# Optimization experiments

Hardware: AMD Instinct MI355X
Metric: run time of the kernel (lower is better)

Reference implementation:

```python
import jax, jax.numpy as jnp
import numpy as np

BS = 8192      # total agents (batch)
T = 8          # trajectory length
NB = 128       # number of sub-batches (crowd groups)
BLK = BS // NB # agents per group = 64
EPS = 1e-7


def setup_inputs() -> dict:
    key = jax.random.key(0)
    ks = jax.random.split(key, 7)
    x = jax.random.normal(ks[0], (BS, T, 2), dtype=jnp.float32)
    # Kaiming-ish scaled params matching nn.Linear fan-in
    W1 = jax.random.normal(ks[1], (2, 32), dtype=jnp.float32) / np.sqrt(2.0)
    b1 = jax.random.normal(ks[2], (32,), dtype=jnp.float32) * 0.01
    W2 = jax.random.normal(ks[3], (32, 64), dtype=jnp.float32) / np.sqrt(32.0)
    b2 = jax.random.normal(ks[4], (64,), dtype=jnp.float32) * 0.01
    W3 = jax.random.normal(ks[5], (64, 64), dtype=jnp.float32) / np.sqrt(64.0)
    b3 = jax.random.normal(ks[6], (64,), dtype=jnp.float32) * 0.01
    starts = jnp.arange(NB, dtype=jnp.int32) * BLK
    sub_batches = jnp.stack([starts, starts + BLK], axis=1)  # [NB, 2]
    return {"x": x, "W1": W1, "b1": b1, "W2": W2, "b2": b2,
            "W3": W3, "b3": b3, "sub_batches": sub_batches}


def reference(x, W1, b1, W2, b2, W3, b3, sub_batches):
    bs = x.shape[0]
    xt = x[:, -1]                                   # [bs, 2] last timestep
    h = jax.nn.relu(xt @ W1 + b1)                   # [bs, 32]
    h = jax.nn.relu(h @ W2 + b2)                    # [bs, 64]
    h = h @ W3 + b3                                 # [bs, 64]

    nb = sub_batches.shape[0]
    blk = bs // nb
    hb = h.reshape(nb, blk, -1)                     # [nb, blk, 64]
    attn = jnp.einsum('nid,njd->nij', hb, hb)       # [nb, blk, blk]
    # Faithful to torch: attn - attn.max(1)[0] broadcasts row-max m[j]
    # along the LAST axis (attn[i,j] - m[j]).
    m = attn.max(axis=2)                            # [nb, blk]
    e = jnp.exp(attn - m[:, None, :])
    blocks = e / (e.sum(axis=2, keepdims=True) + EPS)

    # Scatter normalized blocks onto the block diagonal of a zero bs x bs matrix
    rows = sub_batches[:, 0][:, None] + jnp.arange(blk)  # [nb, blk]
    attens = jnp.zeros((bs, bs), dtype=h.dtype)
    attens = attens.at[rows[:, :, None], rows[:, None, :]].set(blocks)
    return attens
```

## Files before the change

### kernel.cpp

```cpp
#include <hip/hip_runtime.h>

#define BS   8192
#define TT   8
#define NB   128
#define BLK  64
#define EPS  1e-7f

#define FILL_ITERS 16
#define NFILL      ((BS * (BS / 4)) / (256 * FILL_ITERS))

__global__ __launch_bounds__(256, 2) void attn_fused(
    const float* __restrict__ x,
    const float* __restrict__ W1, const float* __restrict__ b1,
    const float* __restrict__ W2, const float* __restrict__ b2,
    const float* __restrict__ W3, const float* __restrict__ b3,
    const int*   __restrict__ sub_batches,
    float* __restrict__ out)
{
    const int tid = threadIdx.x;
    const int bid = blockIdx.x;

    if (bid >= NB) {
        float4* __restrict__ out4 = (float4*)out;
        const float4 z = make_float4(0.f, 0.f, 0.f, 0.f);
        const int base = (bid - NB) * (256 * FILL_ITERS) + tid;
        #pragma unroll
        for (int it = 0; it < FILL_ITERS; ++it) {
            const int idx  = base + it * 256;
            const int row  = idx >> 11;
            const int col4 = idx & 2047;
            if ((col4 >> 4) != (row >> 6)) out4[idx] = z;
        }
        return;
    }

    __shared__ __align__(16) float sW2[32 * 64];
    __shared__ __align__(16) float sW3[64 * 64];
    __shared__ __align__(16) float h1[64][36];
    __shared__ __align__(16) float h2[64][68];
    __shared__ __align__(16) float h3[64][68];
    __shared__ float sW1[2 * 32];
    __shared__ float sb1[32];
    __shared__ float sb2[64];
    __shared__ float sb3[64];
    __shared__ float mcol[64];
    __shared__ float rsum[64][4];

    const int n     = bid;
    const int start = sub_batches[2 * n];

    for (int i = tid; i < 2 * 32; i += 256)  sW1[i] = W1[i];
    if (tid < 32)                            sb1[tid] = b1[tid];
    for (int i = tid; i < 32 * 64; i += 256) sW2[i] = W2[i];
    if (tid < 64)                            sb2[tid] = b2[tid];
    for (int i = tid; i < 64 * 64; i += 256) sW3[i] = W3[i];
    if (tid >= 64 && tid < 128)              sb3[tid - 64] = b3[tid - 64];
    __syncthreads();

    const int row = tid >> 2;
    const int f0  = (tid & 3) * 16;

    const int r = start + row;
    const float2 xv = *(const float2*)&x[((size_t)r * TT + (TT - 1)) * 2];

    {
        const int g0 = (tid & 3) * 8;
        #pragma unroll
        for (int f = 0; f < 8; ++f) {
            float v = fmaf(xv.x, sW1[g0 + f], fmaf(xv.y, sW1[32 + g0 + f], sb1[g0 + f]));
            h1[row][g0 + f] = fmaxf(v, 0.f);
        }
    }
    __syncthreads();

    {
        float acc[16];
        #pragma unroll
        for (int i = 0; i < 16; ++i) acc[i] = sb2[f0 + i];
        for (int k = 0; k < 32; ++k) {
            const float hk = h1[row][k];
            const float4* wp = (const float4*)&sW2[k * 64 + f0];
            #pragma unroll
            for (int c = 0; c < 4; ++c) {
                const float4 w = wp[c];
                acc[4*c+0] = fmaf(hk, w.x, acc[4*c+0]);
                acc[4*c+1] = fmaf(hk, w.y, acc[4*c+1]);
                acc[4*c+2] = fmaf(hk, w.z, acc[4*c+2]);
                acc[4*c+3] = fmaf(hk, w.w, acc[4*c+3]);
            }
        }
        #pragma unroll
        for (int c = 0; c < 4; ++c) {
            float4 v = make_float4(fmaxf(acc[4*c+0], 0.f), fmaxf(acc[4*c+1], 0.f),
                                   fmaxf(acc[4*c+2], 0.f), fmaxf(acc[4*c+3], 0.f));
            ((float4*)&h2[row][f0])[c] = v;
        }
    }
    __syncthreads();

    {
        float acc[16];
        #pragma unroll
        for (int i = 0; i < 16; ++i) acc[i] = sb3[f0 + i];
        for (int k = 0; k < 64; ++k) {
            const float hk = h2[row][k];
            const float4* wp = (const float4*)&sW3[k * 64 + f0];
            #pragma unroll
            for (int c = 0; c < 4; ++c) {
                const float4 w = wp[c];
                acc[4*c+0] = fmaf(hk, w.x, acc[4*c+0]);
                acc[4*c+1] = fmaf(hk, w.y, acc[4*c+1]);
                acc[4*c+2] = fmaf(hk, w.z, acc[4*c+2]);
                acc[4*c+3] = fmaf(hk, w.w, acc[4*c+3]);
            }
        }
        #pragma unroll
        for (int c = 0; c < 4; ++c) {
            ((float4*)&h3[row][f0])[c] =
                make_float4(acc[4*c+0], acc[4*c+1], acc[4*c+2], acc[4*c+3]);
        }
    }
    __syncthreads();

    float (*attn)[68] = h2;
    {
        float4 rv[16];
        const float4* rp = (const float4*)&h3[row][0];
        #pragma unroll
        for (int kk = 0; kk < 16; ++kk) rv[kk] = rp[kk];

        #pragma unroll
        for (int jj = 0; jj < 16; ++jj) {
            const int j = f0 + jj;
            const float4* vp = (const float4*)&h3[j][0];
            float s0 = 0.f, s1 = 0.f, s2 = 0.f, s3 = 0.f;
            #pragma unroll
            for (int kk = 0; kk < 16; ++kk) {
                const float4 v = vp[kk];
                s0 = fmaf(rv[kk].x, v.x, s0);
                s1 = fmaf(rv[kk].y, v.y, s1);
                s2 = fmaf(rv[kk].z, v.z, s2);
                s3 = fmaf(rv[kk].w, v.w, s3);
            }
            attn[row][j] = (s0 + s1) + (s2 + s3);
        }
    }
    __syncthreads();

    if (tid < 64) {
        const float4* ap = (const float4*)&attn[tid][0];
        float4 m4 = ap[0];
        #pragma unroll
        for (int kk = 1; kk < 16; ++kk) {
            const float4 v = ap[kk];
            m4.x = fmaxf(m4.x, v.x); m4.y = fmaxf(m4.y, v.y);
            m4.z = fmaxf(m4.z, v.z); m4.w = fmaxf(m4.w, v.w);
        }
        mcol[tid] = fmaxf(fmaxf(m4.x, m4.y), fmaxf(m4.z, m4.w));
    }
    __syncthreads();

    {
        float ps = 0.f;
        #pragma unroll
        for (int jj = 0; jj < 16; ++jj) {
            const int j = f0 + jj;
            const float e = expf(attn[row][j] - mcol[j]);
            attn[row][j] = e;
            ps += e;
        }
        rsum[row][tid & 3] = ps;
    }
    __syncthreads();

    const float s   = rsum[row][0] + rsum[row][1] + rsum[row][2] + rsum[row][3] + EPS;
    const float inv = 1.f / s;

    float4* ob = (float4*)(out + (size_t)(start + row) * BS + start + f0);
    #pragma unroll
    for (int c = 0; c < 4; ++c) {
        const float4 e4 = ((const float4*)&attn[row][f0])[c];
        ob[c] = make_float4(e4.x * inv, e4.y * inv, e4.z * inv, e4.w * inv);
    }
}

extern "C" void kernel_launch(void* const* d_in, const int* in_sizes, int n_in,
                              void* d_out, int out_size, void* d_ws, size_t ws_size,
                              hipStream_t stream) {
    const float* x   = (const float*)d_in[0];
    const float* W1  = (const float*)d_in[1];
    const float* b1  = (const float*)d_in[2];
    const float* W2  = (const float*)d_in[3];
    const float* b2  = (const float*)d_in[4];
    const float* W3  = (const float*)d_in[5];
    const float* b3  = (const float*)d_in[6];
    const int*   sb  = (const int*)d_in[7];
    float* out = (float*)d_out;

    attn_fused<<<NB + NFILL, 256, 0, stream>>>(x, W1, b1, W2, b2, W3, b3, sb, out);
}
```

Measured before the change: 265.3 us.

## Replace in-kernel zero fill with hipMemsetAsync and widen blocks to 512 threads

Drops the custom fill blocks that wrote zeros off the diagonal and instead clears the whole 256MB output with hipMemsetAsync before launching a block-only kernel. The block kernel now uses 512 threads, with each row split over 8 threads instead of 4, so each thread computes 8 features. This relies on the driver memset reaching full bandwidth, at the cost of writing the diagonal blocks twice and running a second launch serialized on the stream.

```diff
diff --git a/kernel.cpp b/kernel.cpp
--- a/kernel.cpp
+++ b/kernel.cpp
@@ -6,10 +6,7 @@
 #define BLK  64
 #define EPS  1e-7f
 
-#define FILL_ITERS 16
-#define NFILL      ((BS * (BS / 4)) / (256 * FILL_ITERS))
-
-__global__ __launch_bounds__(256, 2) void attn_fused(
+__global__ __launch_bounds__(512) void attn_blocks(
     const float* __restrict__ x,
     const float* __restrict__ W1, const float* __restrict__ b1,
     const float* __restrict__ W2, const float* __restrict__ b2,
@@ -17,23 +14,6 @@
     const int*   __restrict__ sub_batches,
     float* __restrict__ out)
 {
-    const int tid = threadIdx.x;
-    const int bid = blockIdx.x;
-
-    if (bid >= NB) {
-        float4* __restrict__ out4 = (float4*)out;
-        const float4 z = make_float4(0.f, 0.f, 0.f, 0.f);
-        const int base = (bid - NB) * (256 * FILL_ITERS) + tid;
-        #pragma unroll
-        for (int it = 0; it < FILL_ITERS; ++it) {
-            const int idx  = base + it * 256;
-            const int row  = idx >> 11;
-            const int col4 = idx & 2047;
-            if ((col4 >> 4) != (row >> 6)) out4[idx] = z;
-        }
-        return;
-    }
-
     __shared__ __align__(16) float sW2[32 * 64];
     __shared__ __align__(16) float sW3[64 * 64];
     __shared__ __align__(16) float h1[64][36];
@@ -44,29 +24,31 @@
     __shared__ float sb2[64];
     __shared__ float sb3[64];
     __shared__ float mcol[64];
-    __shared__ float rsum[64][4];
+    __shared__ float rsum[64][8];
 
-    const int n     = bid;
+    const int tid   = threadIdx.x;
+    const int n     = blockIdx.x;
     const int start = sub_batches[2 * n];
 
-    for (int i = tid; i < 2 * 32; i += 256)  sW1[i] = W1[i];
+    if (tid < 64)                            sW1[tid] = W1[tid];
     if (tid < 32)                            sb1[tid] = b1[tid];
-    for (int i = tid; i < 32 * 64; i += 256) sW2[i] = W2[i];
-    if (tid < 64)                            sb2[tid] = b2[tid];
-    for (int i = tid; i < 64 * 64; i += 256) sW3[i] = W3[i];
-    if (tid >= 64 && tid < 128)              sb3[tid - 64] = b3[tid - 64];
+    for (int i = tid; i < 32 * 64; i += 512) sW2[i] = W2[i];
+    if (tid >= 448)                          sb2[tid - 448] = b2[tid - 448];
+    for (int i = tid; i < 64 * 64; i += 512) sW3[i] = W3[i];
+    if (tid >= 384 && tid < 448)             sb3[tid - 384] = b3[tid - 384];
     __syncthreads();
 
-    const int row = tid >> 2;
-    const int f0  = (tid & 3) * 16;
+    const int row = tid >> 3;
+    const int l8  = tid & 7;
+    const int f0  = l8 * 8;
 
     const int r = start + row;
     const float2 xv = *(const float2*)&x[((size_t)r * TT + (TT - 1)) * 2];
 
     {
-        const int g0 = (tid & 3) * 8;
+        const int g0 = l8 * 4;
         #pragma unroll
-        for (int f = 0; f < 8; ++f) {
+        for (int f = 0; f < 4; ++f) {
             float v = fmaf(xv.x, sW1[g0 + f], fmaf(xv.y, sW1[32 + g0 + f], sb1[g0 + f]));
             h1[row][g0 + f] = fmaxf(v, 0.f);
         }
@@ -74,14 +56,14 @@
     __syncthreads();
 
     {
-        float acc[16];
+        float acc[8];
         #pragma unroll
-        for (int i = 0; i < 16; ++i) acc[i] = sb2[f0 + i];
+        for (int i = 0; i < 8; ++i) acc[i] = sb2[f0 + i];
         for (int k = 0; k < 32; ++k) {
             const float hk = h1[row][k];
             const float4* wp = (const float4*)&sW2[k * 64 + f0];
             #pragma unroll
-            for (int c = 0; c < 4; ++c) {
+            for (int c = 0; c < 2; ++c) {
                 const float4 w = wp[c];
                 acc[4*c+0] = fmaf(hk, w.x, acc[4*c+0]);
                 acc[4*c+1] = fmaf(hk, w.y, acc[4*c+1]);
@@ -90,23 +72,23 @@
             }
         }
         #pragma unroll
-        for (int c = 0; c < 4; ++c) {
-            float4 v = make_float4(fmaxf(acc[4*c+0], 0.f), fmaxf(acc[4*c+1], 0.f),
-                                   fmaxf(acc[4*c+2], 0.f), fmaxf(acc[4*c+3], 0.f));
-            ((float4*)&h2[row][f0])[c] = v;
+        for (int c = 0; c < 2; ++c) {
+            ((float4*)&h2[row][f0])[c] =
+                make_float4(fmaxf(acc[4*c+0], 0.f), fmaxf(acc[4*c+1], 0.f),
+                            fmaxf(acc[4*c+2], 0.f), fmaxf(acc[4*c+3], 0.f));
         }
     }
     __syncthreads();
 
     {
-        float acc[16];
+        float acc[8];
         #pragma unroll
-        for (int i = 0; i < 16; ++i) acc[i] = sb3[f0 + i];
+        for (int i = 0; i < 8; ++i) acc[i] = sb3[f0 + i];
         for (int k = 0; k < 64; ++k) {
             const float hk = h2[row][k];
             const float4* wp = (const float4*)&sW3[k * 64 + f0];
             #pragma unroll
-            for (int c = 0; c < 4; ++c) {
+            for (int c = 0; c < 2; ++c) {
                 const float4 w = wp[c];
                 acc[4*c+0] = fmaf(hk, w.x, acc[4*c+0]);
                 acc[4*c+1] = fmaf(hk, w.y, acc[4*c+1]);
@@ -115,7 +97,7 @@
             }
         }
         #pragma unroll
-        for (int c = 0; c < 4; ++c) {
+        for (int c = 0; c < 2; ++c) {
             ((float4*)&h3[row][f0])[c] =
                 make_float4(acc[4*c+0], acc[4*c+1], acc[4*c+2], acc[4*c+3]);
         }
@@ -129,8 +111,7 @@
         #pragma unroll
         for (int kk = 0; kk < 16; ++kk) rv[kk] = rp[kk];
 
-        #pragma unroll
-        for (int jj = 0; jj < 16; ++jj) {
+        for (int jj = 0; jj < 8; ++jj) {
             const int j = f0 + jj;
             const float4* vp = (const float4*)&h3[j][0];
             float s0 = 0.f, s1 = 0.f, s2 = 0.f, s3 = 0.f;
@@ -163,22 +144,24 @@
     {
         float ps = 0.f;
         #pragma unroll
-        for (int jj = 0; jj < 16; ++jj) {
+        for (int jj = 0; jj < 8; ++jj) {
             const int j = f0 + jj;
             const float e = expf(attn[row][j] - mcol[j]);
             attn[row][j] = e;
             ps += e;
         }
-        rsum[row][tid & 3] = ps;
+        rsum[row][l8] = ps;
     }
     __syncthreads();
 
-    const float s   = rsum[row][0] + rsum[row][1] + rsum[row][2] + rsum[row][3] + EPS;
+    float s = EPS;
+    #pragma unroll
+    for (int i = 0; i < 8; ++i) s += rsum[row][i];
     const float inv = 1.f / s;
 
     float4* ob = (float4*)(out + (size_t)(start + row) * BS + start + f0);
     #pragma unroll
-    for (int c = 0; c < 4; ++c) {
+    for (int c = 0; c < 2; ++c) {
         const float4 e4 = ((const float4*)&attn[row][f0])[c];
         ob[c] = make_float4(e4.x * inv, e4.y * inv, e4.z * inv, e4.w * inv);
     }
@@ -197,5 +180,7 @@
     const int*   sb  = (const int*)d_in[7];
     float* out = (float*)d_out;
 
-    attn_fused<<<NB + NFILL, 256, 0, stream>>>(x, W1, b1, W2, b2, W3, b3, sb, out);
+    hipMemsetAsync(out, 0, (size_t)BS * BS * sizeof(float), stream);
+
+    attn_blocks<<<NB, 512, 0, stream>>>(x, W1, b1, W2, b2, W3, b3, sb, out);
 }
```

New measurement: 281.9 us. 1.06x slower.
